# Optimization experiments

Hardware: AMD Instinct MI355X
Metric: run time of the kernel (lower is better)

## Reference

```python
import jax, jax.numpy as jnp
import numpy as np

NUM_HEADS = 8
LN_EPS = 1e-5


def _layernorm(x, g, b):
    m = jnp.mean(x, axis=-1, keepdims=True)
    v = jnp.mean(jnp.square(x - m), axis=-1, keepdims=True)
    return (x - m) * jax.lax.rsqrt(v + LN_EPS) * g + b


def setup_inputs() -> dict:
    key = jax.random.key(0)
    ks = jax.random.split(key, 10)
    D, C, Cin = 2, 256, 64  # depth, embed dim, input channels
    w = lambda k, shape: jax.random.normal(k, shape, jnp.float32) * 0.02
    return {
        "x": jax.random.normal(ks[0], (4, Cin, 12, 12, 12), jnp.float32),
        "W_pe": w(ks[1], (Cin, C)),
        "b_pe": jnp.zeros((C,), jnp.float32),
        "cls_token": w(ks[2], (1, 1, C)),
        "ln1_g": jnp.ones((D, C), jnp.float32),
        "ln1_b": jnp.zeros((D, C), jnp.float32),
        "Wqkv": w(ks[3], (D, C, 3 * C)),
        "Wproj": w(ks[4], (D, C, C)),
        "bproj": jnp.zeros((D, C), jnp.float32),
        "ln2_g": jnp.ones((D, C), jnp.float32),
        "ln2_b": jnp.zeros((D, C), jnp.float32),
        "W1": w(ks[5], (D, C, C)),
        "b1": jnp.zeros((D, C), jnp.float32),
        "W2": w(ks[6], (D, C, C)),
        "b2": jnp.zeros((D, C), jnp.float32),
        "normf_g": jnp.ones((C,), jnp.float32),
        "normf_b": jnp.zeros((C,), jnp.float32),
    }


def reference(x, W_pe, b_pe, cls_token, ln1_g, ln1_b, Wqkv, Wproj, bproj,
              ln2_g, ln2_b, W1, b1, W2, b2, normf_g, normf_b):
    B, Cin, H, W, L = x.shape
    C = W_pe.shape[1]
    hd = C // NUM_HEADS
    scale = hd ** (-0.5)

    # PatchEmbed: 1x1x1 Conv3d == per-voxel linear projection, then flatten to tokens
    tok = jnp.einsum('bchwl,cd->bhwld', x, W_pe).reshape(B, H * W * L, C) + b_pe
    cls = jnp.broadcast_to(cls_token, (B, 1, C))
    t = jnp.concatenate([cls, tok], axis=1)  # [B, N, C], N = H*W*L + 1
    N = t.shape[1]

    depth = Wqkv.shape[0]
    for i in range(depth):
        # --- self-attention ---
        y = _layernorm(t, ln1_g[i], ln1_b[i])
        qkv = (y @ Wqkv[i]).reshape(B, N, 3, NUM_HEADS, hd)
        qkv = jnp.transpose(qkv, (2, 0, 3, 1, 4))  # [3, B, H, N, hd]
        q, k, v = qkv[0], qkv[1], qkv[2]
        attn = jnp.einsum('bhnd,bhmd->bhnm', q, k) * scale
        attn = jax.nn.softmax(attn, axis=-1)
        o = jnp.einsum('bhnm,bhmd->bhnd', attn, v)
        o = jnp.transpose(o, (0, 2, 1, 3)).reshape(B, N, C)
        t = t + (o @ Wproj[i] + bproj[i])
        # --- MLP (mlp_ratio=1.0, exact GELU) ---
        y = _layernorm(t, ln2_g[i], ln2_b[i])
        h = jax.nn.gelu(y @ W1[i] + b1[i], approximate=False)
        t = t + (h @ W2[i] + b2[i])

    t = _layernorm(t, normf_g, normf_b)
    x_cls = t[:, 0]                                   # [B, C]
    feat = t[:, 1:]                                   # [B, H*W*L, C]
    feat = jnp.transpose(feat, (0, 2, 1)).reshape(B, C, H, W, L)  # downsample = Identity for dim=256
    return x_cls, feat
```

## Files before the change

### kernel.cpp

```cpp
#include <hip/hip_runtime.h>
#include <hip/hip_bf16.h>
#include <math.h>

#define B_   4
#define CIN  64
#define P_   1728
#define N_   1729
#define C_   256
#define NH_  8
#define HD_  32
#define M_   (B_*N_)
#define NPAD 1792
#define NB_EMBED 6916

typedef __bf16 bf16x8 __attribute__((ext_vector_type(8)));
typedef __bf16 bf16x4 __attribute__((ext_vector_type(4)));
typedef float  f32x4  __attribute__((ext_vector_type(4)));
typedef float  f32x16 __attribute__((ext_vector_type(16)));

__global__ __launch_bounds__(256) void embed3(
    const float* __restrict__ x, const float* __restrict__ Wpe,
    const float* __restrict__ bpe, const float* __restrict__ cls,
    float* __restrict__ t, __bf16* __restrict__ kB, __bf16* __restrict__ vB,
    float* __restrict__ stats)
{
    if (blockIdx.x >= NB_EMBED) {
        int ex = blockIdx.x - NB_EMBED;
        if (ex < 252) {
            int idx = ex*256 + threadIdx.x;
            if (idx < 32*63*32) {
                int d  = idx & 31;
                int n  = (idx >> 5) % 63 + N_;
                int bh = idx / (63*32);
                kB[((size_t)bh*NPAD + n)*32 + d] = (__bf16)0.f;
                vB[((size_t)bh*32 + d)*NPAD + n] = (__bf16)0.f;
            }
        } else {
            int si = (ex - 252)*256 + threadIdx.x;
            if (si < 2*M_) stats[si] = 0.f;
        }
        return;
    }
    int idx = blockIdx.x*256 + threadIdx.x;
    int c   = idx & 255;
    int n   = (idx >> 8) % N_;
    int b   = idx / (N_*256);
    if (n == 0) { t[idx] = cls[c]; return; }
    int p = n - 1;
    float acc = bpe[c];
    for (int ci = 0; ci < CIN; ++ci)
        acc += x[(size_t)(b*CIN + ci)*P_ + p] * Wpe[ci*C_ + c];
    t[idx] = acc;
}

__global__ __launch_bounds__(256) void ln4(
    const float* __restrict__ in, __bf16* __restrict__ out,
    const float* __restrict__ g, const float* __restrict__ bb)
{
    int wv = threadIdx.x >> 6, lane = threadIdx.x & 63;
    size_t row = (size_t)blockIdx.x*4 + wv;
    float4 v = *(const float4*)&in[row*C_ + lane*4];
    float s1 = (v.x+v.y)+(v.z+v.w);
    float s2 = (v.x*v.x+v.y*v.y)+(v.z*v.z+v.w*v.w);
    #pragma unroll
    for (int off = 32; off >= 1; off >>= 1) {
        s1 += __shfl_xor(s1, off);
        s2 += __shfl_xor(s2, off);
    }
    float mean = s1*(1.0f/C_);
    float var  = fmaxf(s2*(1.0f/C_) - mean*mean, 0.0f);
    float rstd = rsqrtf(var + 1e-5f);
    float4 gg = *(const float4*)&g[lane*4];
    float4 bv = *(const float4*)&bb[lane*4];
    bf16x4 r;
    r[0] = (__bf16)((v.x-mean)*rstd*gg.x + bv.x);
    r[1] = (__bf16)((v.y-mean)*rstd*gg.y + bv.y);
    r[2] = (__bf16)((v.z-mean)*rstd*gg.z + bv.z);
    r[3] = (__bf16)((v.w-mean)*rstd*gg.w + bv.w);
    *(bf16x4*)&out[row*C_ + lane*4] = r;
}

__global__ __launch_bounds__(256) void wprep2(
    const float* __restrict__ Wqkv, const float* __restrict__ Wproj,
    const float* __restrict__ W1,   const float* __restrict__ W2,
    __bf16* __restrict__ wT)
{
    int z = blockIdx.z, which = z >> 1, layer = z & 1;
    const float* src; __bf16* dst; int NC;
    if (which == 0) {
        src = Wqkv + (size_t)layer*C_*768;
        dst = wT   + (size_t)layer*768*256;
        NC  = 768;
    } else {
        NC = 256;
        const float* b3 = (which == 1) ? Wproj : (which == 2) ? W1 : W2;
        src = b3 + (size_t)layer*65536;
        dst = wT + 2*768*256 + (size_t)((which-1)*2 + layer)*65536;
    }
    int n0 = blockIdx.x*32; if (n0 >= NC) return;
    int k0 = blockIdx.y*32;
    __shared__ float tile[32][33];
    int c = threadIdx.x & 31, r = threadIdx.x >> 5;
    for (int rr = r; rr < 32; rr += 8)
        tile[rr][c] = src[(size_t)(k0+rr)*NC + n0 + c];
    __syncthreads();
    for (int rr = r; rr < 32; rr += 8)
        dst[(size_t)(n0+rr)*256 + k0 + c] = (__bf16)tile[c][rr];
}

template<int NC, bool ADD, bool GELU, bool BIAS, bool OUTBF, bool STATS>
__global__ __launch_bounds__(256) void gemm4(
    const __bf16* __restrict__ A, const __bf16* __restrict__ Wt,
    const float* __restrict__ bias, float* __restrict__ outF,
    __bf16* __restrict__ outB, float* __restrict__ stats)
{
    __shared__ __align__(16) __bf16 As[2][64*64];
    __shared__ __align__(16) __bf16 Bs[2][64*64];
    int r0 = blockIdx.x*64, c0 = blockIdx.y*64;
    int tid = threadIdx.x;
    int wv = tid >> 6, lane = tid & 63, quad = lane >> 4, mn = lane & 15;
    int sr = tid >> 2, sc = tid & 3;
    int ga = r0 + sr; if (ga >= M_) ga = M_ - 1;

    f32x4 acc[4];
    #pragma unroll
    for (int ct = 0; ct < 4; ++ct)
        #pragma unroll
        for (int rr = 0; rr < 4; ++rr) acc[ct][rr] = 0.f;

    bf16x8 ra0, ra1, rb0, rb1;
#define GLOAD(KC) do {                                                   \
        ra0 = *(const bf16x8*)&A[(size_t)ga*256 + (KC)*64 + sc*8];       \
        ra1 = *(const bf16x8*)&A[(size_t)ga*256 + (KC)*64 + sc*8 + 32];  \
        rb0 = *(const bf16x8*)&Wt[(size_t)(c0+sr)*256 + (KC)*64 + sc*8]; \
        rb1 = *(const bf16x8*)&Wt[(size_t)(c0+sr)*256 + (KC)*64 + sc*8 + 32]; \
    } while (0)
#define SSTORE(BUF) do {                                                 \
        *(bf16x8*)&As[BUF][sr*64 + ((sc ^ (sr & 7))*8)]       = ra0;     \
        *(bf16x8*)&As[BUF][sr*64 + (((sc+4) ^ (sr & 7))*8)]   = ra1;     \
        *(bf16x8*)&Bs[BUF][sr*64 + ((sc ^ (sr & 7))*8)]       = rb0;     \
        *(bf16x8*)&Bs[BUF][sr*64 + (((sc+4) ^ (sr & 7))*8)]   = rb1;     \
    } while (0)

    GLOAD(0);
    SSTORE(0);
    __syncthreads();

    for (int kc = 0; kc < 4; ++kc) {
        int cur = kc & 1;
        if (kc < 3) GLOAD(kc+1);
        __builtin_amdgcn_sched_barrier(0);

        #pragma unroll
        for (int h = 0; h < 2; ++h) {
            bf16x8 a = *(const bf16x8*)&As[cur][(wv*16 + mn)*64 + (((h*4+quad) ^ (mn & 7))*8)];
            #pragma unroll
            for (int ct = 0; ct < 4; ++ct) {
                bf16x8 b = *(const bf16x8*)&Bs[cur][(ct*16 + mn)*64 + (((h*4+quad) ^ (mn & 7))*8)];
                acc[ct] = __builtin_amdgcn_mfma_f32_16x16x32_bf16(a, b, acc[ct], 0, 0, 0);
            }
        }

        if (kc < 3) {
            SSTORE(cur^1);
            __syncthreads();
        }
    }
#undef GLOAD
#undef SSTORE

    float rs1[4] = {0.f,0.f,0.f,0.f}, rs2[4] = {0.f,0.f,0.f,0.f};
    #pragma unroll
    for (int ct = 0; ct < 4; ++ct) {
        int col = c0 + ct*16 + mn;
        #pragma unroll
        for (int rr = 0; rr < 4; ++rr) {
            int row = r0 + wv*16 + quad*4 + rr;
            if (row >= M_) continue;
            float val = acc[ct][rr];
            if (BIAS) val += bias[col];
            if (GELU) val = 0.5f*val*(1.f + erff(val*0.70710678118654752f));
            size_t oi = (size_t)row*NC + col;
            if (OUTBF) outB[oi] = (__bf16)val;
            else if (ADD) {
                float tv = outF[oi] + val;
                outF[oi] = tv;
                if (STATS) { rs1[rr] += tv; rs2[rr] += tv*tv; }
            }
            else outF[oi] = val;
        }
    }
    if (STATS) {
        #pragma unroll
        for (int rr = 0; rr < 4; ++rr) {
            float s1 = rs1[rr], s2 = rs2[rr];
            s1 += __shfl_xor(s1, 1); s1 += __shfl_xor(s1, 2);
            s1 += __shfl_xor(s1, 4); s1 += __shfl_xor(s1, 8);
            s2 += __shfl_xor(s2, 1); s2 += __shfl_xor(s2, 2);
            s2 += __shfl_xor(s2, 4); s2 += __shfl_xor(s2, 8);
            int row = r0 + wv*16 + quad*4 + rr;
            if (mn == 0 && row < M_) {
                atomicAdd(&stats[2*row],     s1);
                atomicAdd(&stats[2*row + 1], s2);
            }
        }
    }
}

__global__ __launch_bounds__(256) void gemm_qkv4(
    const __bf16* __restrict__ A, const __bf16* __restrict__ Wt,
    __bf16* __restrict__ qB, __bf16* __restrict__ kB, __bf16* __restrict__ vB)
{
    __shared__ __align__(16) __bf16 As[2][64*64];
    __shared__ __align__(16) __bf16 Bs[2][64*64];
    int r0 = blockIdx.x*64, c0 = blockIdx.y*64;
    int tid = threadIdx.x;
    int wv = tid >> 6, lane = tid & 63, quad = lane >> 4, mn = lane & 15;
    int sr = tid >> 2, sc = tid & 3;
    int ga = r0 + sr; if (ga >= M_) ga = M_ - 1;

    f32x4 acc[4];
    #pragma unroll
    for (int ct = 0; ct < 4; ++ct)
        #pragma unroll
        for (int rr = 0; rr < 4; ++rr) acc[ct][rr] = 0.f;

    bf16x8 ra0, ra1, rb0, rb1;
#define GLOAD(KC) do {                                                   \
        ra0 = *(const bf16x8*)&A[(size_t)ga*256 + (KC)*64 + sc*8];       \
        ra1 = *(const bf16x8*)&A[(size_t)ga*256 + (KC)*64 + sc*8 + 32];  \
        rb0 = *(const bf16x8*)&Wt[(size_t)(c0+sr)*256 + (KC)*64 + sc*8]; \
        rb1 = *(const bf16x8*)&Wt[(size_t)(c0+sr)*256 + (KC)*64 + sc*8 + 32]; \
    } while (0)
#define SSTORE(BUF) do {                                                 \
        *(bf16x8*)&As[BUF][sr*64 + ((sc ^ (sr & 7))*8)]       = ra0;     \
        *(bf16x8*)&As[BUF][sr*64 + (((sc+4) ^ (sr & 7))*8)]   = ra1;     \
        *(bf16x8*)&Bs[BUF][sr*64 + ((sc ^ (sr & 7))*8)]       = rb0;     \
        *(bf16x8*)&Bs[BUF][sr*64 + (((sc+4) ^ (sr & 7))*8)]   = rb1;     \
    } while (0)

    GLOAD(0);
    SSTORE(0);
    __syncthreads();

    for (int kc = 0; kc < 4; ++kc) {
        int cur = kc & 1;
        if (kc < 3) GLOAD(kc+1);
        __builtin_amdgcn_sched_barrier(0);

        #pragma unroll
        for (int h = 0; h < 2; ++h) {
            bf16x8 a = *(const bf16x8*)&As[cur][(wv*16 + mn)*64 + (((h*4+quad) ^ (mn & 7))*8)];
            #pragma unroll
            for (int ct = 0; ct < 4; ++ct) {
                bf16x8 b = *(const bf16x8*)&Bs[cur][(ct*16 + mn)*64 + (((h*4+quad) ^ (mn & 7))*8)];
                acc[ct] = __builtin_amdgcn_mfma_f32_16x16x32_bf16(a, b, acc[ct], 0, 0, 0);
            }
        }

        if (kc < 3) {
            SSTORE(cur^1);
            __syncthreads();
        }
    }
#undef GLOAD
#undef SSTORE

    const float scale = 0.2550348727f;
    #pragma unroll
    for (int ct = 0; ct < 4; ++ct) {
        int col = c0 + ct*16 + mn;
        #pragma unroll
        for (int rr = 0; rr < 4; ++rr) {
            int row = r0 + wv*16 + quad*4 + rr;
            if (row >= M_) continue;
            int b = row / N_, n = row - b*N_;
            float val = acc[ct][rr];
            if (col < 256) {
                int h = col >> 5, dd = col & 31;
                qB[((size_t)(b*NH_+h)*NPAD + n)*32 + dd] = (__bf16)(val*scale);
            } else if (col < 512) {
                int h = (col-256) >> 5, dd = col & 31;
                kB[((size_t)(b*NH_+h)*NPAD + n)*32 + dd] = (__bf16)val;
            } else {
                int h = (col-512) >> 5, dd = col & 31;
                vB[((size_t)(b*NH_+h)*32 + dd)*NPAD + n] = (__bf16)val;
            }
        }
    }
}

#define LKS 40
#define LVS 136

__device__ __forceinline__ float fexp2(float x) {
    float r; asm("v_exp_f32 %0, %1" : "=v"(r) : "v"(x)); return r;
}
__device__ __forceinline__ unsigned cvtpk_bf16(float lo, float hi) {
    unsigned r;
    asm("v_cvt_pk_bf16_f32 %0, %1, %2" : "=v"(r) : "v"(lo), "v"(hi));
    return r;
}

__global__ __launch_bounds__(128) void attn13(
    const __bf16* __restrict__ qB, const __bf16* __restrict__ kB,
    const __bf16* __restrict__ vB, __bf16* __restrict__ o)
{
    int bh = blockIdx.x, b = bh >> 3, h = bh & 7;
    int q0 = blockIdx.y * 64;
    int tid = threadIdx.x;
    int wv = tid >> 6, lane = tid & 63, lo5 = lane & 31, hi = lane >> 5;

    __shared__ __align__(16) __bf16 lk[2][128*LKS];
    __shared__ __align__(16) __bf16 lvt[2][32*LVS];

    const __bf16* kbase = kB + (size_t)bh*NPAD*32;
    const __bf16* vbase = vB + (size_t)bh*32*NPAD;

    const __bf16* qrow = qB + ((size_t)bh*NPAD + q0 + wv*32 + lo5)*32 + hi*8;
    bf16x8 qf0 = *(const bf16x8*)(qrow);
    bf16x8 qf1 = *(const bf16x8*)(qrow + 16);

    f32x16 oaccA, oaccB;
    #pragma unroll
    for (int r = 0; r < 16; ++r) { oaccA[r] = 0.f; oaccB[r] = 0.f; }
    float lsum = 0.f;

    int vr = tid >> 2, vc = tid & 3;

    bf16x8 ks0, ks1, ks2, ks3, vs0, vs1, vs2, vs3;
#define ATTN_LOAD(T) do {                                              \
        const __bf16* kp_ = kbase + ((size_t)((T)*128 + tid))*32;      \
        ks0 = *(const bf16x8*)(kp_);                                   \
        ks1 = *(const bf16x8*)(kp_ + 8);                               \
        ks2 = *(const bf16x8*)(kp_ + 16);                              \
        ks3 = *(const bf16x8*)(kp_ + 24);                              \
        const __bf16* vp_ = vbase + (size_t)vr*NPAD + (T)*128 + vc*32; \
        vs0 = *(const bf16x8*)(vp_);                                   \
        vs1 = *(const bf16x8*)(vp_ + 8);                               \
        vs2 = *(const bf16x8*)(vp_ + 16);                              \
        vs3 = *(const bf16x8*)(vp_ + 24);                              \
    } while (0)
#define ATTN_STORE(BUF) do {                                           \
        __bf16* kd = &lk[BUF][tid*LKS];                                \
        *(bf16x8*)(kd)      = ks0;  *(bf16x8*)(kd + 8)  = ks1;         \
        *(bf16x8*)(kd + 16) = ks2;  *(bf16x8*)(kd + 24) = ks3;         \
        __bf16* vd = &lvt[BUF][vr*LVS + vc*32];                        \
        *(bf16x8*)(vd)      = vs0;  *(bf16x8*)(vd + 8)  = vs1;         \
        *(bf16x8*)(vd + 16) = vs2;  *(bf16x8*)(vd + 24) = vs3;         \
    } while (0)

    ATTN_LOAD(0);
    ATTN_STORE(0);
    __syncthreads();

    for (int t = 0; t < 14; ++t) {
        int cur = t & 1;
        if (t < 13) ATTN_LOAD(t+1);
        __builtin_amdgcn_sched_barrier(0);

        f32x16 s[4];
        __builtin_amdgcn_s_setprio(1);
        #pragma unroll
        for (int kg = 0; kg < 4; ++kg) {
            const __bf16* kf = &lk[cur][(kg*32 + lo5)*LKS + hi*8];
            bf16x8 kf0 = *(const bf16x8*)(kf);
            bf16x8 kf1 = *(const bf16x8*)(kf + 16);
            #pragma unroll
            for (int r = 0; r < 16; ++r) s[kg][r] = 0.f;
            s[kg] = __builtin_amdgcn_mfma_f32_32x32x16_bf16(kf0, qf0, s[kg], 0, 0, 0);
            s[kg] = __builtin_amdgcn_mfma_f32_32x32x16_bf16(kf1, qf1, s[kg], 0, 0, 0);
        }
        __builtin_amdgcn_s_setprio(0);

        #pragma unroll
        for (int kg = 0; kg < 4; ++kg) {
            float p[16];
            #pragma unroll
            for (int r = 0; r < 16; ++r) p[r] = fexp2(s[kg][r]);
            float l0 = 0.f, l1 = 0.f;
            #pragma unroll
            for (int r = 0; r < 8; ++r) { l0 += p[r]; l1 += p[r+8]; }
            lsum += l0 + l1;

            unsigned a0 = cvtpk_bf16(p[0],  p[1]),  a1 = cvtpk_bf16(p[2],  p[3]);
            unsigned b0 = cvtpk_bf16(p[4],  p[5]),  b1 = cvtpk_bf16(p[6],  p[7]);
            unsigned c0 = cvtpk_bf16(p[8],  p[9]),  c1 = cvtpk_bf16(p[10], p[11]);
            unsigned d0 = cvtpk_bf16(p[12], p[13]), d1 = cvtpk_bf16(p[14], p[15]);
            asm("v_permlane32_swap_b32 %0, %1" : "+v"(a0), "+v"(b0));
            asm("v_permlane32_swap_b32 %0, %1" : "+v"(a1), "+v"(b1));
            asm("v_permlane32_swap_b32 %0, %1" : "+v"(c0), "+v"(d0));
            asm("v_permlane32_swap_b32 %0, %1" : "+v"(c1), "+v"(d1));
            union { bf16x8 v; unsigned u[4]; } f0, f1;
            f0.u[0] = a0; f0.u[1] = a1; f0.u[2] = b0; f0.u[3] = b1;
            f1.u[0] = c0; f1.u[1] = c1; f1.u[2] = d0; f1.u[3] = d1;

            const __bf16* vf = &lvt[cur][lo5*LVS + kg*32 + hi*8];
            bf16x8 vf0 = *(const bf16x8*)(vf);
            bf16x8 vf1 = *(const bf16x8*)(vf + 16);
            __builtin_amdgcn_s_setprio(1);
            if (kg & 1) {
                oaccB = __builtin_amdgcn_mfma_f32_32x32x16_bf16(f0.v, vf0, oaccB, 0, 0, 0);
                oaccB = __builtin_amdgcn_mfma_f32_32x32x16_bf16(f1.v, vf1, oaccB, 0, 0, 0);
            } else {
                oaccA = __builtin_amdgcn_mfma_f32_32x32x16_bf16(f0.v, vf0, oaccA, 0, 0, 0);
                oaccA = __builtin_amdgcn_mfma_f32_32x32x16_bf16(f1.v, vf1, oaccA, 0, 0, 0);
            }
            __builtin_amdgcn_s_setprio(0);
        }

        if (t < 13) {
            ATTN_STORE(cur^1);
            __syncthreads();
        }
    }
#undef ATTN_LOAD
#undef ATTN_STORE

    lsum += __shfl_xor(lsum, 32);
    float inv = 1.0f / (lsum - 63.0f);

    #pragma unroll
    for (int r = 0; r < 16; ++r) {
        float oa = oaccA[r] + oaccB[r];
        int qrw = (r & 3) + 8*(r >> 2) + 4*hi;
        float li = __shfl(inv, qrw);
        int q = q0 + wv*32 + qrw;
        if (q < N_)
            o[((size_t)b*N_ + q)*C_ + h*HD_ + lo5] = (__bf16)(oa * li);
    }
}

__global__ __launch_bounds__(256) void featln(
    const float* __restrict__ t, const float* __restrict__ stats,
    const float* __restrict__ g, const float* __restrict__ bb,
    float* __restrict__ out_cls, float* __restrict__ out_feat)
{
    int bx = blockIdx.x;
    if (bx == 54) {
        if (blockIdx.y != 0) return;
        int b = blockIdx.z, c = threadIdx.x;
        size_t row = (size_t)b*N_;
        float s1 = stats[2*row], s2 = stats[2*row+1];
        float mean = s1*(1.0f/C_);
        float rstd = rsqrtf(fmaxf(s2*(1.0f/C_) - mean*mean, 0.0f) + 1e-5f);
        out_cls[b*C_ + c] = (t[row*C_ + c] - mean)*rstd*g[c] + bb[c];
        return;
    }
    __shared__ float tl[32][33];
    int p0 = bx*32, c0 = blockIdx.y*32, b = blockIdx.z;
    int cc = threadIdx.x & 31, rr = threadIdx.x >> 5;
    float gg = g[c0+cc], bv = bb[c0+cc];
    for (int i = rr; i < 32; i += 8) {
        size_t row = (size_t)b*N_ + 1 + p0 + i;
        float s1 = stats[2*row], s2 = stats[2*row+1];
        float mean = s1*(1.0f/C_);
        float rstd = rsqrtf(fmaxf(s2*(1.0f/C_) - mean*mean, 0.0f) + 1e-5f);
        tl[i][cc] = (t[row*C_ + c0 + cc] - mean)*rstd*gg + bv;
    }
    __syncthreads();
    for (int i = rr; i < 32; i += 8)
        out_feat[((size_t)(b*C_) + c0 + i)*P_ + p0 + cc] = tl[cc][i];
}

extern "C" void kernel_launch(void* const* d_in, const int* in_sizes, int n_in,
                              void* d_out, int out_size, void* d_ws, size_t ws_size,
                              hipStream_t stream)
{
    const float* x        = (const float*)d_in[0];
    const float* W_pe     = (const float*)d_in[1];
    const float* b_pe     = (const float*)d_in[2];
    const float* cls_tok  = (const float*)d_in[3];
    const float* ln1_g    = (const float*)d_in[4];
    const float* ln1_b    = (const float*)d_in[5];
    const float* Wqkv     = (const float*)d_in[6];
    const float* Wproj    = (const float*)d_in[7];
    const float* bproj    = (const float*)d_in[8];
    const float* ln2_g    = (const float*)d_in[9];
    const float* ln2_b    = (const float*)d_in[10];
    const float* W1       = (const float*)d_in[11];
    const float* b1       = (const float*)d_in[12];
    const float* W2       = (const float*)d_in[13];
    const float* b2       = (const float*)d_in[14];
    const float* normf_g  = (const float*)d_in[15];
    const float* normf_b  = (const float*)d_in[16];

    const size_t MC = (size_t)M_*C_;
    float*  ws  = (float*)d_ws;
    float*  t   = ws;
    float*  stats = ws + MC;
    __bf16* ybf = (__bf16*)(ws + 2*MC);
    __bf16* hbf = (__bf16*)(ws + 2*MC + MC/2);
    __bf16* obf = (__bf16*)(ws + 2*MC + MC);
    __bf16* wT  = (__bf16*)(ws + 2*MC + 3*(MC/2));
    __bf16* qB  = wT + 2*768*256 + 6*256*256;
    __bf16* kB  = qB + (size_t)B_*NH_*NPAD*32;
    __bf16* vB  = kB + (size_t)B_*NH_*NPAD*32;

    __bf16* projT = wT + 2*768*256;
    __bf16* w1T   = projT + 2*256*256;
    __bf16* w2T   = w1T   + 2*256*256;

    float* out_cls  = (float*)d_out;
    float* out_feat = out_cls + B_*C_;

    wprep2<<<dim3(24, 8, 8), 256, 0, stream>>>(Wqkv, Wproj, W1, W2, wT);
    embed3<<<NB_EMBED + 252 + 55, 256, 0, stream>>>(
        x, W_pe, b_pe, cls_tok, t, kB, vB, stats);

    const int GRID_M = (M_ + 63) / 64;
    for (int i = 0; i < 2; ++i) {
        ln4<<<M_/4, 256, 0, stream>>>(t, ybf, ln1_g + i*C_, ln1_b + i*C_);
        gemm_qkv4<<<dim3(GRID_M, 12), 256, 0, stream>>>(
            ybf, wT + (size_t)i*768*256, qB, kB, vB);
        attn13<<<dim3(32, 28), 128, 0, stream>>>(qB, kB, vB, obf);
        gemm4<256,true,false,true,false,false><<<dim3(GRID_M, 4), 256, 0, stream>>>(
            obf, projT + (size_t)i*65536, bproj + i*C_, t, nullptr, nullptr);
        ln4<<<M_/4, 256, 0, stream>>>(t, ybf, ln2_g + i*C_, ln2_b + i*C_);
        gemm4<256,false,true,true,true,false><<<dim3(GRID_M, 4), 256, 0, stream>>>(
            ybf, w1T + (size_t)i*65536, b1 + i*C_, nullptr, hbf, nullptr);
        if (i == 0)
            gemm4<256,true,false,true,false,false><<<dim3(GRID_M, 4), 256, 0, stream>>>(
                hbf, w2T + (size_t)i*65536, b2 + i*C_, t, nullptr, nullptr);
        else
            gemm4<256,true,false,true,false,true><<<dim3(GRID_M, 4), 256, 0, stream>>>(
                hbf, w2T + (size_t)i*65536, b2 + i*C_, t, nullptr, stats);
    }

    featln<<<dim3(55, 8, 4), 256, 0, stream>>>(
        t, stats, normf_g, normf_b, out_cls, out_feat);
}
```

Measured before the change: 282.5 us.

## Fold LayerNorm into following GEMMs via precomputed stats and weight corrections

Measured after the change: 304.8 us. 7.9% more time.

```diff
diff --git a/kernel.cpp b/kernel.cpp
--- a/kernel.cpp
+++ b/kernel.cpp
@@ -11,78 +11,51 @@
 #define HD_  32
 #define M_   (B_*N_)
 #define NPAD 1792
-#define NB_EMBED 6916
+#define STB  (2*M_)
 
 typedef __bf16 bf16x8 __attribute__((ext_vector_type(8)));
 typedef __bf16 bf16x4 __attribute__((ext_vector_type(4)));
 typedef float  f32x4  __attribute__((ext_vector_type(4)));
 typedef float  f32x16 __attribute__((ext_vector_type(16)));
 
-__global__ __launch_bounds__(256) void embed3(
-    const float* __restrict__ x, const float* __restrict__ Wpe,
-    const float* __restrict__ bpe, const float* __restrict__ cls,
-    float* __restrict__ t, __bf16* __restrict__ kB, __bf16* __restrict__ vB,
-    float* __restrict__ stats)
-{
-    if (blockIdx.x >= NB_EMBED) {
-        int ex = blockIdx.x - NB_EMBED;
-        if (ex < 252) {
-            int idx = ex*256 + threadIdx.x;
-            if (idx < 32*63*32) {
-                int d  = idx & 31;
-                int n  = (idx >> 5) % 63 + N_;
-                int bh = idx / (63*32);
-                kB[((size_t)bh*NPAD + n)*32 + d] = (__bf16)0.f;
-                vB[((size_t)bh*32 + d)*NPAD + n] = (__bf16)0.f;
-            }
-        } else {
-            int si = (ex - 252)*256 + threadIdx.x;
-            if (si < 2*M_) stats[si] = 0.f;
-        }
-        return;
-    }
-    int idx = blockIdx.x*256 + threadIdx.x;
-    int c   = idx & 255;
-    int n   = (idx >> 8) % N_;
-    int b   = idx / (N_*256);
-    if (n == 0) { t[idx] = cls[c]; return; }
-    int p = n - 1;
-    float acc = bpe[c];
-    for (int ci = 0; ci < CIN; ++ci)
-        acc += x[(size_t)(b*CIN + ci)*P_ + p] * Wpe[ci*C_ + c];
-    t[idx] = acc;
-}
-
-__global__ __launch_bounds__(256) void ln4(
-    const float* __restrict__ in, __bf16* __restrict__ out,
-    const float* __restrict__ g, const float* __restrict__ bb)
-{
-    int wv = threadIdx.x >> 6, lane = threadIdx.x & 63;
-    size_t row = (size_t)blockIdx.x*4 + wv;
-    float4 v = *(const float4*)&in[row*C_ + lane*4];
-    float s1 = (v.x+v.y)+(v.z+v.w);
-    float s2 = (v.x*v.x+v.y*v.y)+(v.z*v.z+v.w*v.w);
-    #pragma unroll
-    for (int off = 32; off >= 1; off >>= 1) {
-        s1 += __shfl_xor(s1, off);
-        s2 += __shfl_xor(s2, off);
-    }
-    float mean = s1*(1.0f/C_);
-    float var  = fmaxf(s2*(1.0f/C_) - mean*mean, 0.0f);
-    float rstd = rsqrtf(var + 1e-5f);
-    float4 gg = *(const float4*)&g[lane*4];
-    float4 bv = *(const float4*)&bb[lane*4];
-    bf16x4 r;
-    r[0] = (__bf16)((v.x-mean)*rstd*gg.x + bv.x);
-    r[1] = (__bf16)((v.y-mean)*rstd*gg.y + bv.y);
-    r[2] = (__bf16)((v.z-mean)*rstd*gg.z + bv.z);
-    r[3] = (__bf16)((v.w-mean)*rstd*gg.w + bv.w);
-    *(bf16x4*)&out[row*C_ + lane*4] = r;
-}
-
-__global__ __launch_bounds__(256) void wprep2(
+__global__ __launch_bounds__(256) void lnprep(
+    const float* __restrict__ Wqkv, const float* __restrict__ W1,
+    const float* __restrict__ ln1_g, const float* __restrict__ ln1_b,
+    const float* __restrict__ ln2_g, const float* __restrict__ ln2_b,
+    float* __restrict__ lnc)
+{
+    int gid = blockIdx.x*256 + threadIdx.x;
+    if (gid >= 2048) return;
+    int l = gid >> 10, n = gid & 1023;
+    float cw = 0.f, bw = 0.f;
+    if (n < 768) {
+        const float* W = Wqkv + (size_t)l*C_*768;
+        const float* g = ln1_g + l*C_;
+        const float* b = ln1_b + l*C_;
+        for (int k = 0; k < C_; ++k) {
+            float w = W[(size_t)k*768 + n];
+            cw += g[k]*w; bw += b[k]*w;
+        }
+        lnc[l*2048 + n]       = cw;
+        lnc[l*2048 + 768 + n] = bw;
+    } else {
+        int nn = n - 768;
+        const float* W = W1 + (size_t)l*C_*C_;
+        const float* g = ln2_g + l*C_;
+        const float* b = ln2_b + l*C_;
+        for (int k = 0; k < C_; ++k) {
+            float w = W[(size_t)k*C_ + nn];
+            cw += g[k]*w; bw += b[k]*w;
+        }
+        lnc[l*2048 + 1536 + nn] = cw;
+        lnc[l*2048 + 1792 + nn] = bw;
+    }
+}
+
+__global__ __launch_bounds__(256) void wprep3(
     const float* __restrict__ Wqkv, const float* __restrict__ Wproj,
     const float* __restrict__ W1,   const float* __restrict__ W2,
+    const float* __restrict__ ln1_g, const float* __restrict__ ln2_g,
     __bf16* __restrict__ wT)
 {
     int z = blockIdx.z, which = z >> 1, layer = z & 1;
@@ -104,15 +77,74 @@
     for (int rr = r; rr < 32; rr += 8)
         tile[rr][c] = src[(size_t)(k0+rr)*NC + n0 + c];
     __syncthreads();
+    float gs = 1.f;
+    if (which == 0) gs = ln1_g[layer*C_ + k0 + c];
+    else if (which == 2) gs = ln2_g[layer*C_ + k0 + c];
     for (int rr = r; rr < 32; rr += 8)
-        dst[(size_t)(n0+rr)*256 + k0 + c] = (__bf16)tile[c][rr];
-}
-
-template<int NC, bool ADD, bool GELU, bool BIAS, bool OUTBF, bool STATS>
-__global__ __launch_bounds__(256) void gemm4(
+        dst[(size_t)(n0+rr)*256 + k0 + c] = (__bf16)(tile[c][rr] * gs);
+}
+
+__global__ __launch_bounds__(256) void embed4(
+    const float* __restrict__ x, const float* __restrict__ Wpe,
+    const float* __restrict__ bpe, const float* __restrict__ cls,
+    float* __restrict__ t, __bf16* __restrict__ tbf,
+    __bf16* __restrict__ kB, __bf16* __restrict__ vB,
+    float* __restrict__ stats)
+{
+    __shared__ float rs[8];
+    if (blockIdx.x >= M_) {
+        int ex = blockIdx.x - M_;
+        if (ex < 252) {
+            int idx = ex*256 + threadIdx.x;
+            if (idx < 32*63*32) {
+                int d  = idx & 31;
+                int n  = (idx >> 5) % 63 + N_;
+                int bh = idx / (63*32);
+                kB[((size_t)bh*NPAD + n)*32 + d] = (__bf16)0.f;
+                vB[((size_t)bh*32 + d)*NPAD + n] = (__bf16)0.f;
+            }
+        } else {
+            int si = (ex - 252)*256 + threadIdx.x;
+            if (si < 4*STB) stats[STB + si] = 0.f;
+        }
+        return;
+    }
+    int row = blockIdx.x;
+    int b = row / N_, n = row - b*N_;
+    int c = threadIdx.x;
+    float val;
+    if (n == 0) val = cls[c];
+    else {
+        int p = n - 1;
+        val = bpe[c];
+        for (int ci = 0; ci < CIN; ++ci)
+            val += x[(size_t)(b*CIN + ci)*P_ + p] * Wpe[ci*C_ + c];
+    }
+    t[(size_t)row*C_ + c]   = val;
+    tbf[(size_t)row*C_ + c] = (__bf16)val;
+
+    float s1 = val, s2 = val*val;
+    #pragma unroll
+    for (int off = 32; off >= 1; off >>= 1) {
+        s1 += __shfl_xor(s1, off);
+        s2 += __shfl_xor(s2, off);
+    }
+    int wvi = c >> 6;
+    if ((c & 63) == 0) { rs[wvi] = s1; rs[wvi+4] = s2; }
+    __syncthreads();
+    if (c == 0) {
+        stats[2*(size_t)row]     = rs[0]+rs[1]+rs[2]+rs[3];
+        stats[2*(size_t)row + 1] = rs[4]+rs[5]+rs[6]+rs[7];
+    }
+}
+
+template<bool GELU, bool BIAS, bool OUTBF, bool ADD, bool STATS, bool LNFIX, bool TBF>
+__global__ __launch_bounds__(256) void gemm6(
     const __bf16* __restrict__ A, const __bf16* __restrict__ Wt,
     const float* __restrict__ bias, float* __restrict__ outF,
-    __bf16* __restrict__ outB, float* __restrict__ stats)
+    __bf16* __restrict__ outB, __bf16* __restrict__ tbfo,
+    float* __restrict__ statso, const float* __restrict__ statsi,
+    const float* __restrict__ cw, const float* __restrict__ bw)
 {
     __shared__ __align__(16) __bf16 As[2][64*64];
     __shared__ __align__(16) __bf16 Bs[2][64*64];
@@ -169,22 +201,37 @@
 #undef GLOAD
 #undef SSTORE
 
+    float mean4[4], rstd4[4];
+    if (LNFIX) {
+        #pragma unroll
+        for (int rr = 0; rr < 4; ++rr) {
+            int row = r0 + wv*16 + quad*4 + rr; if (row >= M_) row = M_-1;
+            float s1 = statsi[2*row], s2 = statsi[2*row+1];
+            float mn_ = s1*(1.0f/C_);
+            mean4[rr] = mn_;
+            rstd4[rr] = rsqrtf(fmaxf(s2*(1.0f/C_) - mn_*mn_, 0.0f) + 1e-5f);
+        }
+    }
     float rs1[4] = {0.f,0.f,0.f,0.f}, rs2[4] = {0.f,0.f,0.f,0.f};
     #pragma unroll
     for (int ct = 0; ct < 4; ++ct) {
         int col = c0 + ct*16 + mn;
+        float cwv = 0.f, bwv = 0.f;
+        if (LNFIX) { cwv = cw[col]; bwv = bw[col]; }
         #pragma unroll
         for (int rr = 0; rr < 4; ++rr) {
             int row = r0 + wv*16 + quad*4 + rr;
             if (row >= M_) continue;
             float val = acc[ct][rr];
+            if (LNFIX) val = rstd4[rr]*(val - mean4[rr]*cwv) + bwv;
             if (BIAS) val += bias[col];
             if (GELU) val = 0.5f*val*(1.f + erff(val*0.70710678118654752f));
-            size_t oi = (size_t)row*NC + col;
+            size_t oi = (size_t)row*C_ + col;
             if (OUTBF) outB[oi] = (__bf16)val;
             else if (ADD) {
                 float tv = outF[oi] + val;
                 outF[oi] = tv;
+                if (TBF) tbfo[oi] = (__bf16)tv;
                 if (STATS) { rs1[rr] += tv; rs2[rr] += tv*tv; }
             }
             else outF[oi] = val;
@@ -200,15 +247,16 @@
             s2 += __shfl_xor(s2, 4); s2 += __shfl_xor(s2, 8);
             int row = r0 + wv*16 + quad*4 + rr;
             if (mn == 0 && row < M_) {
-                atomicAdd(&stats[2*row],     s1);
-                atomicAdd(&stats[2*row + 1], s2);
-            }
-        }
-    }
-}
-
-__global__ __launch_bounds__(256) void gemm_qkv4(
+                atomicAdd(&statso[2*row],     s1);
+                atomicAdd(&statso[2*row + 1], s2);
+            }
+        }
+    }
+}
+
+__global__ __launch_bounds__(256) void gemm_qkv6(
     const __bf16* __restrict__ A, const __bf16* __restrict__ Wt,
+    const float* __restrict__ statsi, const float* __restrict__ lncl,
     __bf16* __restrict__ qB, __bf16* __restrict__ kB, __bf16* __restrict__ vB)
 {
     __shared__ __align__(16) __bf16 As[2][64*64];
@@ -266,19 +314,30 @@
 #undef GLOAD
 #undef SSTORE
 
-    const float scale = 0.2550348727f;
+    float mean4[4], rstd4[4];
+    #pragma unroll
+    for (int rr = 0; rr < 4; ++rr) {
+        int row = r0 + wv*16 + quad*4 + rr; if (row >= M_) row = M_-1;
+        float s1 = statsi[2*row], s2 = statsi[2*row+1];
+        float mn_ = s1*(1.0f/C_);
+        mean4[rr] = mn_;
+        rstd4[rr] = rsqrtf(fmaxf(s2*(1.0f/C_) - mn_*mn_, 0.0f) + 1e-5f);
+    }
+
+    const float qsc = 0.2550348727f;
     #pragma unroll
     for (int ct = 0; ct < 4; ++ct) {
         int col = c0 + ct*16 + mn;
+        float cwv = lncl[col], bwv = lncl[768 + col];
         #pragma unroll
         for (int rr = 0; rr < 4; ++rr) {
             int row = r0 + wv*16 + quad*4 + rr;
             if (row >= M_) continue;
             int b = row / N_, n = row - b*N_;
-            float val = acc[ct][rr];
+            float val = rstd4[rr]*(acc[ct][rr] - mean4[rr]*cwv) + bwv;
             if (col < 256) {
                 int h = col >> 5, dd = col & 31;
-                qB[((size_t)(b*NH_+h)*NPAD + n)*32 + dd] = (__bf16)(val*scale);
+                qB[((size_t)(b*NH_+h)*NPAD + n)*32 + dd] = (__bf16)(val*qsc);
             } else if (col < 512) {
                 int h = (col-256) >> 5, dd = col & 31;
                 kB[((size_t)(b*NH_+h)*NPAD + n)*32 + dd] = (__bf16)val;
@@ -486,16 +545,17 @@
     const float* normf_b  = (const float*)d_in[16];
 
     const size_t MC = (size_t)M_*C_;
-    float*  ws  = (float*)d_ws;
-    float*  t   = ws;
+    float*  ws    = (float*)d_ws;
+    float*  t     = ws;
     float*  stats = ws + MC;
-    __bf16* ybf = (__bf16*)(ws + 2*MC);
-    __bf16* hbf = (__bf16*)(ws + 2*MC + MC/2);
-    __bf16* obf = (__bf16*)(ws + 2*MC + MC);
-    __bf16* wT  = (__bf16*)(ws + 2*MC + 3*(MC/2));
-    __bf16* qB  = wT + 2*768*256 + 6*256*256;
-    __bf16* kB  = qB + (size_t)B_*NH_*NPAD*32;
-    __bf16* vB  = kB + (size_t)B_*NH_*NPAD*32;
+    float*  lnc   = stats + 5*STB + 88;
+    __bf16* tbf   = (__bf16*)(lnc + 4096);
+    __bf16* hbf   = tbf + MC;
+    __bf16* obf   = hbf + MC;
+    __bf16* wT    = obf + MC;
+    __bf16* qB    = wT + 2*768*256 + 6*256*256;
+    __bf16* kB    = qB + (size_t)B_*NH_*NPAD*32;
+    __bf16* vB    = kB + (size_t)B_*NH_*NPAD*32;
 
     __bf16* projT = wT + 2*768*256;
     __bf16* w1T   = projT + 2*256*256;
@@ -504,29 +564,30 @@
     float* out_cls  = (float*)d_out;
     float* out_feat = out_cls + B_*C_;
 
-    wprep2<<<dim3(24, 8, 8), 256, 0, stream>>>(Wqkv, Wproj, W1, W2, wT);
-    embed3<<<NB_EMBED + 252 + 55, 256, 0, stream>>>(
-        x, W_pe, b_pe, cls_tok, t, kB, vB, stats);
+    wprep3<<<dim3(24, 8, 8), 256, 0, stream>>>(
+        Wqkv, Wproj, W1, W2, ln1_g, ln2_g, wT);
+    lnprep<<<8, 256, 0, stream>>>(Wqkv, W1, ln1_g, ln1_b, ln2_g, ln2_b, lnc);
+    embed4<<<M_ + 252 + 217, 256, 0, stream>>>(
+        x, W_pe, b_pe, cls_tok, t, tbf, kB, vB, stats);
 
     const int GRID_M = (M_ + 63) / 64;
     for (int i = 0; i < 2; ++i) {
-        ln4<<<M_/4, 256, 0, stream>>>(t, ybf, ln1_g + i*C_, ln1_b + i*C_);
-        gemm_qkv4<<<dim3(GRID_M, 12), 256, 0, stream>>>(
-            ybf, wT + (size_t)i*768*256, qB, kB, vB);
+        gemm_qkv6<<<dim3(GRID_M, 12), 256, 0, stream>>>(
+            tbf, wT + (size_t)i*768*256,
+            stats + (i ? 2 : 0)*STB, lnc + i*2048, qB, kB, vB);
         attn13<<<dim3(32, 28), 128, 0, stream>>>(qB, kB, vB, obf);
-        gemm4<256,true,false,true,false,false><<<dim3(GRID_M, 4), 256, 0, stream>>>(
-            obf, projT + (size_t)i*65536, bproj + i*C_, t, nullptr, nullptr);
-        ln4<<<M_/4, 256, 0, stream>>>(t, ybf, ln2_g + i*C_, ln2_b + i*C_);
-        gemm4<256,false,true,true,true,false><<<dim3(GRID_M, 4), 256, 0, stream>>>(
-            ybf, w1T + (size_t)i*65536, b1 + i*C_, nullptr, hbf, nullptr);
-        if (i == 0)
-            gemm4<256,true,false,true,false,false><<<dim3(GRID_M, 4), 256, 0, stream>>>(
-                hbf, w2T + (size_t)i*65536, b2 + i*C_, t, nullptr, nullptr);
-        else
-            gemm4<256,true,false,true,false,true><<<dim3(GRID_M, 4), 256, 0, stream>>>(
-                hbf, w2T + (size_t)i*65536, b2 + i*C_, t, nullptr, stats);
+        gemm6<false,true,false,true,true,false,true><<<dim3(GRID_M, 4), 256, 0, stream>>>(
+            obf, projT + (size_t)i*65536, bproj + i*C_, t, nullptr, tbf,
+            stats + (i ? 3 : 1)*STB, nullptr, nullptr, nullptr);
+        gemm6<true,true,true,false,false,true,false><<<dim3(GRID_M, 4), 256, 0, stream>>>(
+            tbf, w1T + (size_t)i*65536, b1 + i*C_, nullptr, hbf, nullptr,
+            nullptr, stats + (i ? 3 : 1)*STB,
+            lnc + i*2048 + 1536, lnc + i*2048 + 1792);
+        gemm6<false,true,false,true,true,false,true><<<dim3(GRID_M, 4), 256, 0, stream>>>(
+            hbf, w2T + (size_t)i*65536, b2 + i*C_, t, nullptr, tbf,
+            stats + (i ? 4 : 2)*STB, nullptr, nullptr, nullptr);
     }
 
     featln<<<dim3(55, 8, 4), 256, 0, stream>>>(
-        t, stats, normf_g, normf_b, out_cls, out_feat);
-}
+        t, stats + 4*STB, normf_g, normf_b, out_cls, out_feat);
+}
```
